# Optimization experiments

Measured on AMD Instinct MI355X. Metric: run time of the kernel, lower is better.

Reference implementation:

```python
import jax, jax.numpy as jnp
import numpy as np

N, E = 20000, 320000
NODE_DIM, HID, HEADS, OUT = 256, 64, 4, 50
NEG_SLOPE = 0.2  # PyG GATv2Conv default
BN_EPS = 1e-5


def setup_inputs() -> dict:
    key = jax.random.key(0)
    ks = jax.random.split(key, 16)
    s = 0.05
    inp = {
        'x': jax.random.normal(ks[0], (N, NODE_DIM), dtype=jnp.float32),
        'edge_index': jax.random.randint(ks[1], (2, E), 0, N, dtype=jnp.int64),
        # GATv2 layer 1: in=NODE_DIM, out=HID, heads=HEADS, concat
        'W1l': jax.random.normal(ks[2], (NODE_DIM, HEADS * HID), dtype=jnp.float32) * s,
        'W1r': jax.random.normal(ks[3], (NODE_DIM, HEADS * HID), dtype=jnp.float32) * s,
        'att1': jax.random.normal(ks[4], (HEADS, HID), dtype=jnp.float32) * s,
        'b1': jnp.zeros((HEADS * HID,), dtype=jnp.float32),
        'bn1_g': jnp.ones((HEADS * HID,), dtype=jnp.float32),
        'bn1_b': jnp.zeros((HEADS * HID,), dtype=jnp.float32),
        # GATv2 layer 2: in=HEADS*HID, out=HID, heads=1
        'W2l': jax.random.normal(ks[5], (HEADS * HID, HID), dtype=jnp.float32) * s,
        'W2r': jax.random.normal(ks[6], (HEADS * HID, HID), dtype=jnp.float32) * s,
        'att2': jax.random.normal(ks[7], (1, HID), dtype=jnp.float32) * s,
        'b2': jnp.zeros((HID,), dtype=jnp.float32),
        'bn2_g': jnp.ones((HID,), dtype=jnp.float32),
        'bn2_b': jnp.zeros((HID,), dtype=jnp.float32),
        # class head
        'Wc': jax.random.normal(ks[8], (HID, OUT), dtype=jnp.float32) * s,
        'bc': jnp.zeros((OUT,), dtype=jnp.float32),
    }
    return inp


def gatv2(x, src, dst, Wl, Wr, att, bias, heads, d):
    n = x.shape[0]
    xl = (x @ Wl).reshape(n, heads, d)  # source-side transform (messages)
    xr = (x @ Wr).reshape(n, heads, d)  # target-side transform
    xj = xl[src]                        # [E, H, D] gathered source feats
    xi = xr[dst]                        # [E, H, D] gathered target feats
    e = jax.nn.leaky_relu(xi + xj, NEG_SLOPE)
    score = jnp.einsum('ehd,hd->eh', e, att)   # [E, H]
    # segment softmax over incoming edges of each destination node
    m = jax.ops.segment_max(score, dst, num_segments=n)         # [N, H]
    m = jnp.where(jnp.isfinite(m), m, 0.0)
    p = jnp.exp(score - m[dst])
    denom = jax.ops.segment_sum(p, dst, num_segments=n)          # [N, H]
    alpha = p / (denom[dst] + 1e-16)
    out = jax.ops.segment_sum(alpha[:, :, None] * xj, dst, num_segments=n)  # [N, H, D]
    return out.reshape(n, heads * d) + bias


def batchnorm(x, gamma, beta):
    mu = jnp.mean(x, axis=0)
    var = jnp.var(x, axis=0)
    return (x - mu) * jax.lax.rsqrt(var + BN_EPS) * gamma + beta


def reference(x, edge_index, W1l, W1r, att1, b1, bn1_g, bn1_b,
              W2l, W2r, att2, b2, bn2_g, bn2_b, Wc, bc):
    src, dst = edge_index[0], edge_index[1]
    h = gatv2(x, src, dst, W1l, W1r, att1, b1, HEADS, HID)
    h = jax.nn.gelu(batchnorm(h, bn1_g, bn1_b), approximate=False)
    h = gatv2(h, src, dst, W2l, W2r, att2, b2, 1, HID)
    h = jax.nn.gelu(batchnorm(h, bn2_g, bn2_b), approximate=False)
    return jax.nn.log_softmax(h @ Wc + bc, axis=1)
```

## Files before the change

### kernel.cpp

```cpp
#include <hip/hip_runtime.h>
#include <math.h>

#define N_NODES 20000
#define N_EDGES 320000
#define NODE_DIM 256
#define HID 64
#define HEADS 4
#define OUTC 50
#define NEG_SLOPE 0.2f
#define BN_EPS 1e-5f

typedef __attribute__((ext_vector_type(8))) short short8;
typedef __attribute__((ext_vector_type(8))) unsigned short ushort8;
typedef __attribute__((ext_vector_type(4))) unsigned short ushort4v;
typedef __attribute__((ext_vector_type(4))) float f32x4;

__device__ inline unsigned short f2bf(float f) {
  unsigned u = __float_as_uint(f);
  u += 0x7fffu + ((u >> 16) & 1u);
  return (unsigned short)(u >> 16);
}

__device__ inline float bf2f(unsigned short u) {
  return __uint_as_float((unsigned)u << 16);
}

__device__ inline float gelu_exact(float v) {
  return 0.5f * v * (1.f + erff(v * 0.70710678118f));
}

__global__ void cast_f32_bf16_kernel(const float* __restrict__ in,
                                     unsigned short* __restrict__ out, int n4) {
  int i = blockIdx.x * blockDim.x + threadIdx.x;
  if (i >= n4) return;
  float4 v = ((const float4*)in)[i];
  ushort4v o = {f2bf(v.x), f2bf(v.y), f2bf(v.z), f2bf(v.w)};
  ((ushort4v*)out)[i] = o;
}

__global__ void cast_weights_kernel(const float* __restrict__ W1l, const float* __restrict__ W1r,
                                    const float* __restrict__ W2l, const float* __restrict__ W2r,
                                    unsigned short* __restrict__ w1b,
                                    unsigned short* __restrict__ w2b) {
  int i = blockIdx.x * blockDim.x + threadIdx.x;
  if (i < 131072) {
    int k = i >> 9, j = i & 511;
    w1b[i] = f2bf(j < 256 ? W1l[k * 256 + j] : W1r[k * 256 + j - 256]);
  }
  if (i < 32768) {
    int k = i >> 7, j = i & 127;
    w2b[i] = f2bf(j < 64 ? W2l[k * 64 + j] : W2r[k * 64 + j - 64]);
  }
}

__global__ __launch_bounds__(256) void gemm_bf16_kernel(
    const unsigned short* __restrict__ A, const unsigned short* __restrict__ B,
    unsigned short* __restrict__ C, int M, int K, int N) {
  __shared__ unsigned short As[128][40];
  __shared__ unsigned short Bs[64][40];
  int tid = threadIdx.x;
  int lane = tid & 63, w = tid >> 6;
  int bm = blockIdx.y * 128, bn = blockIdx.x * 64;

  f32x4 acc[2][4] = {};

  for (int k0 = 0; k0 < K; k0 += 32) {
#pragma unroll
    for (int s = tid; s < 512; s += 256) {
      int row = s >> 2, half = s & 3;
      int gr = bm + row;
      ushort8 v = {0, 0, 0, 0, 0, 0, 0, 0};
      if (gr < M) v = *(const ushort8*)&A[(size_t)gr * K + k0 + half * 8];
      *(ushort8*)&As[row][half * 8] = v;
    }
    {
      int k = tid >> 3, c0 = (tid & 7) * 8;
      ushort8 v = *(const ushort8*)&B[(size_t)(k0 + k) * N + bn + c0];
#pragma unroll
      for (int j = 0; j < 8; j++) Bs[c0 + j][k] = v[j];
    }
    __syncthreads();

    short8 av[2], bv[4];
#pragma unroll
    for (int fr = 0; fr < 2; fr++)
      av[fr] = *(const short8*)&As[w * 32 + fr * 16 + (lane & 15)][(lane >> 4) * 8];
#pragma unroll
    for (int fc = 0; fc < 4; fc++)
      bv[fc] = *(const short8*)&Bs[fc * 16 + (lane & 15)][(lane >> 4) * 8];
#pragma unroll
    for (int fr = 0; fr < 2; fr++)
#pragma unroll
      for (int fc = 0; fc < 4; fc++)
        acc[fr][fc] = __builtin_amdgcn_mfma_f32_16x16x32_bf16(av[fr], bv[fc], acc[fr][fc], 0, 0, 0);
    __syncthreads();
  }

#pragma unroll
  for (int fr = 0; fr < 2; fr++)
#pragma unroll
    for (int fc = 0; fc < 4; fc++)
#pragma unroll
      for (int i = 0; i < 4; i++) {
        int r = bm + w * 32 + fr * 16 + (lane >> 4) * 4 + i;
        if (r < M) C[(size_t)r * N + bn + fc * 16 + (lane & 15)] = f2bf(acc[fr][fc][i]);
      }
}

__global__ void hist_kernel(const int* __restrict__ dst, int* __restrict__ deg) {
  int i = blockIdx.x * blockDim.x + threadIdx.x;
  if (i < N_EDGES) atomicAdd(&deg[dst[i]], 1);
}

__global__ void scan_kernel(const int* __restrict__ deg, int* __restrict__ rowptr) {
  __shared__ int part[1024];
  int tid = threadIdx.x;
  const int CH = (N_NODES + 1023) / 1024;
  int base = tid * CH;
  int s = 0;
  for (int i = 0; i < CH; i++) {
    int idx = base + i;
    if (idx < N_NODES) s += deg[idx];
  }
  part[tid] = s;
  __syncthreads();
  for (int off = 1; off < 1024; off <<= 1) {
    int v = (tid >= off) ? part[tid - off] : 0;
    __syncthreads();
    part[tid] += v;
    __syncthreads();
  }
  int run = (tid == 0) ? 0 : part[tid - 1];
  for (int i = 0; i < CH; i++) {
    int idx = base + i;
    if (idx < N_NODES) {
      rowptr[idx] = run;
      run += deg[idx];
    }
  }
  if (tid == 1023) rowptr[N_NODES] = run;
}

__global__ void scatter_kernel(const int* __restrict__ src, const int* __restrict__ dst,
                               const int* __restrict__ rowptr, int* __restrict__ cursor,
                               int* __restrict__ csr_src) {
  int i = blockIdx.x * blockDim.x + threadIdx.x;
  if (i < N_EDGES) {
    int d = dst[i];
    int pos = rowptr[d] + atomicAdd(&cursor[d], 1);
    csr_src[pos] = src[i];
  }
}

__global__ void agg1_kernel(const unsigned short* __restrict__ C1,
                            const float* __restrict__ att, const float* __restrict__ bias,
                            const int* __restrict__ rowptr, const int* __restrict__ csr_src,
                            float* __restrict__ out) {
  int wave = threadIdx.x >> 6;
  int lane = threadIdx.x & 63;
  int n = blockIdx.x * 4 + wave;
  if (n >= N_NODES) return;

  ushort4v xi4 = *(const ushort4v*)&C1[(size_t)n * 512 + 256 + 4 * lane];
  float xi0 = bf2f(xi4[0]), xi1 = bf2f(xi4[1]), xi2 = bf2f(xi4[2]), xi3 = bf2f(xi4[3]);
  float4 attv = *(const float4*)&att[4 * lane];

  float acc0 = 0.f, acc1 = 0.f, acc2 = 0.f, acc3 = 0.f;
  float lsum = 0.f;

  int e0 = rowptr[n], e1 = rowptr[n + 1];
  int e = e0;
  for (; e + 2 <= e1; e += 2) {
    int s0 = csr_src[e];
    int s1 = csr_src[e + 1];
    ushort4v a4 = *(const ushort4v*)&C1[(size_t)s0 * 512 + 4 * lane];
    ushort4v b4 = *(const ushort4v*)&C1[(size_t)s1 * 512 + 4 * lane];
    float xa0 = bf2f(a4[0]), xa1 = bf2f(a4[1]), xa2 = bf2f(a4[2]), xa3 = bf2f(a4[3]);
    float xb0 = bf2f(b4[0]), xb1 = bf2f(b4[1]), xb2 = bf2f(b4[2]), xb3 = bf2f(b4[3]);

    float ua0 = xi0 + xa0, ua1 = xi1 + xa1, ua2 = xi2 + xa2, ua3 = xi3 + xa3;
    float ub0 = xi0 + xb0, ub1 = xi1 + xb1, ub2 = xi2 + xb2, ub3 = xi3 + xb3;
    float ta = fmaxf(ua0, NEG_SLOPE * ua0) * attv.x + fmaxf(ua1, NEG_SLOPE * ua1) * attv.y +
               fmaxf(ua2, NEG_SLOPE * ua2) * attv.z + fmaxf(ua3, NEG_SLOPE * ua3) * attv.w;
    float tb = fmaxf(ub0, NEG_SLOPE * ub0) * attv.x + fmaxf(ub1, NEG_SLOPE * ub1) * attv.y +
               fmaxf(ub2, NEG_SLOPE * ub2) * attv.z + fmaxf(ub3, NEG_SLOPE * ub3) * attv.w;

    ta += __shfl_xor(ta, 8);  tb += __shfl_xor(tb, 8);
    ta += __shfl_xor(ta, 4);  tb += __shfl_xor(tb, 4);
    ta += __shfl_xor(ta, 2);  tb += __shfl_xor(tb, 2);
    ta += __shfl_xor(ta, 1);  tb += __shfl_xor(tb, 1);

    float pa = expf(ta);
    float pb = expf(tb);
    lsum += pa + pb;
    acc0 += pa * xa0 + pb * xb0;
    acc1 += pa * xa1 + pb * xb1;
    acc2 += pa * xa2 + pb * xb2;
    acc3 += pa * xa3 + pb * xb3;
  }
  if (e < e1) {
    int s0 = csr_src[e];
    ushort4v a4 = *(const ushort4v*)&C1[(size_t)s0 * 512 + 4 * lane];
    float xa0 = bf2f(a4[0]), xa1 = bf2f(a4[1]), xa2 = bf2f(a4[2]), xa3 = bf2f(a4[3]);
    float ua0 = xi0 + xa0, ua1 = xi1 + xa1, ua2 = xi2 + xa2, ua3 = xi3 + xa3;
    float ta = fmaxf(ua0, NEG_SLOPE * ua0) * attv.x + fmaxf(ua1, NEG_SLOPE * ua1) * attv.y +
               fmaxf(ua2, NEG_SLOPE * ua2) * attv.z + fmaxf(ua3, NEG_SLOPE * ua3) * attv.w;
    ta += __shfl_xor(ta, 8);
    ta += __shfl_xor(ta, 4);
    ta += __shfl_xor(ta, 2);
    ta += __shfl_xor(ta, 1);
    float pa = expf(ta);
    lsum += pa;
    acc0 += pa * xa0;
    acc1 += pa * xa1;
    acc2 += pa * xa2;
    acc3 += pa * xa3;
  }

  float inv = 1.f / (lsum + 1e-16f);
  float4 bv = *(const float4*)&bias[4 * lane];
  float4 o;
  o.x = acc0 * inv + bv.x;
  o.y = acc1 * inv + bv.y;
  o.z = acc2 * inv + bv.z;
  o.w = acc3 * inv + bv.w;
  *(float4*)&out[(size_t)n * 256 + 4 * lane] = o;
}

__global__ void agg2_kernel(const unsigned short* __restrict__ xlr,
                            const float* __restrict__ att, const float* __restrict__ bias,
                            const int* __restrict__ rowptr, const int* __restrict__ csr_src,
                            float* __restrict__ out) {
  int wave = threadIdx.x >> 6;
  int lane = threadIdx.x & 63;
  int n = blockIdx.x * 4 + wave;
  if (n >= N_NODES) return;

  int g = lane >> 4, slot = lane & 15;
  ushort4v xi4 = *(const ushort4v*)&xlr[(size_t)n * 128 + 64 + 4 * slot];
  float xi0 = bf2f(xi4[0]), xi1 = bf2f(xi4[1]), xi2 = bf2f(xi4[2]), xi3 = bf2f(xi4[3]);
  float4 attv = *(const float4*)&att[4 * slot];

  float acc0 = 0.f, acc1 = 0.f, acc2 = 0.f, acc3 = 0.f;
  float lsum = 0.f;

  int e0 = rowptr[n], e1 = rowptr[n + 1];
  int nt = (e1 - e0 + 3) >> 2;
  for (int it = 0; it < nt; it++) {
    int e = e0 + it * 4 + g;
    bool valid = e < e1;
    int s = valid ? csr_src[e] : 0;
    ushort4v xj4 = *(const ushort4v*)&xlr[(size_t)s * 128 + 4 * slot];
    float xj0 = bf2f(xj4[0]), xj1 = bf2f(xj4[1]), xj2 = bf2f(xj4[2]), xj3 = bf2f(xj4[3]);
    float u0 = xi0 + xj0, u1 = xi1 + xj1, u2 = xi2 + xj2, u3 = xi3 + xj3;
    float t = fmaxf(u0, NEG_SLOPE * u0) * attv.x + fmaxf(u1, NEG_SLOPE * u1) * attv.y +
              fmaxf(u2, NEG_SLOPE * u2) * attv.z + fmaxf(u3, NEG_SLOPE * u3) * attv.w;
    t += __shfl_xor(t, 8);
    t += __shfl_xor(t, 4);
    t += __shfl_xor(t, 2);
    t += __shfl_xor(t, 1);
    float p = valid ? expf(t) : 0.f;
    lsum += p;
    acc0 += p * xj0;
    acc1 += p * xj1;
    acc2 += p * xj2;
    acc3 += p * xj3;
  }

  acc0 += __shfl_xor(acc0, 16); acc0 += __shfl_xor(acc0, 32);
  acc1 += __shfl_xor(acc1, 16); acc1 += __shfl_xor(acc1, 32);
  acc2 += __shfl_xor(acc2, 16); acc2 += __shfl_xor(acc2, 32);
  acc3 += __shfl_xor(acc3, 16); acc3 += __shfl_xor(acc3, 32);
  lsum += __shfl_xor(lsum, 16); lsum += __shfl_xor(lsum, 32);

  if (g == 0) {
    float inv = 1.f / (lsum + 1e-16f);
    float4 bv = *(const float4*)&bias[4 * slot];
    float4 o;
    o.x = acc0 * inv + bv.x;
    o.y = acc1 * inv + bv.y;
    o.z = acc2 * inv + bv.z;
    o.w = acc3 * inv + bv.w;
    *(float4*)&out[(size_t)n * 64 + 4 * slot] = o;
  }
}

__global__ void bn_stage1_256_kernel(const float* __restrict__ x, float* __restrict__ partial) {
  int c = threadIdx.x;
  int r0 = blockIdx.x * 84;
  int r1 = min(r0 + 84, N_NODES);
  float s = 0.f, q = 0.f;
  for (int r = r0; r < r1; r++) {
    float v = x[(size_t)r * 256 + c];
    s += v;
    q += v * v;
  }
  partial[(size_t)blockIdx.x * 512 + c] = s;
  partial[(size_t)blockIdx.x * 512 + 256 + c] = q;
}

__global__ void bn_stage1_64_kernel(const float* __restrict__ x, float* __restrict__ partial) {
  __shared__ float ls[256], lq[256];
  int tid = threadIdx.x;
  int c = tid & 63, g = tid >> 6;
  int r0 = blockIdx.x * 84 + g;
  int r1 = min(blockIdx.x * 84 + 84, N_NODES);
  float s = 0.f, q = 0.f;
  for (int r = r0; r < r1; r += 4) {
    float v = x[(size_t)r * 64 + c];
    s += v;
    q += v * v;
  }
  ls[tid] = s;
  lq[tid] = q;
  __syncthreads();
  if (g == 0) {
    s += ls[64 + c] + ls[128 + c] + ls[192 + c];
    q += lq[64 + c] + lq[128 + c] + lq[192 + c];
    partial[(size_t)blockIdx.x * 128 + c] = s;
    partial[(size_t)blockIdx.x * 128 + 64 + c] = q;
  }
}

__global__ void bn_stage2_kernel(const float* __restrict__ partial, int C,
                                 const float* __restrict__ gamma, const float* __restrict__ beta,
                                 float* __restrict__ ss) {
  int c = threadIdx.x;
  if (c >= C) return;
  float s = 0.f, q = 0.f;
  for (int b = 0; b < 240; b++) {
    s += partial[(size_t)b * 2 * C + c];
    q += partial[(size_t)b * 2 * C + C + c];
  }
  float mu = s * (1.0f / N_NODES);
  float var = q * (1.0f / N_NODES) - mu * mu;
  float sc = gamma[c] * rsqrtf(var + BN_EPS);
  ss[c] = sc;
  ss[C + c] = beta[c] - mu * sc;
}

__global__ void bn_gelu1_kernel(const float* __restrict__ x, const float* __restrict__ ss,
                                unsigned short* __restrict__ y) {
  const int total4 = N_NODES * 256 / 4;
  for (int i = blockIdx.x * blockDim.x + threadIdx.x; i < total4;
       i += gridDim.x * blockDim.x) {
    int c0 = (i & 63) * 4;
    float4 v = ((const float4*)x)[i];
    float a0 = gelu_exact(v.x * ss[c0 + 0] + ss[256 + c0 + 0]);
    float a1 = gelu_exact(v.y * ss[c0 + 1] + ss[256 + c0 + 1]);
    float a2 = gelu_exact(v.z * ss[c0 + 2] + ss[256 + c0 + 2]);
    float a3 = gelu_exact(v.w * ss[c0 + 3] + ss[256 + c0 + 3]);
    ushort4v o = {f2bf(a0), f2bf(a1), f2bf(a2), f2bf(a3)};
    ((ushort4v*)y)[i] = o;
  }
}

__global__ void bn_gelu2_kernel(const float* __restrict__ x, const float* __restrict__ ss,
                                float* __restrict__ y) {
  const int total4 = N_NODES * 64 / 4;
  for (int i = blockIdx.x * blockDim.x + threadIdx.x; i < total4;
       i += gridDim.x * blockDim.x) {
    int c0 = (i & 15) * 4;
    float4 v = ((const float4*)x)[i];
    float4 o;
    o.x = gelu_exact(v.x * ss[c0 + 0] + ss[64 + c0 + 0]);
    o.y = gelu_exact(v.y * ss[c0 + 1] + ss[64 + c0 + 1]);
    o.z = gelu_exact(v.z * ss[c0 + 2] + ss[64 + c0 + 2]);
    o.w = gelu_exact(v.w * ss[c0 + 3] + ss[64 + c0 + 3]);
    ((float4*)y)[i] = o;
  }
}

__global__ void head_kernel(const float* __restrict__ h, const float* __restrict__ Wc,
                            const float* __restrict__ bc, float* __restrict__ out) {
  __shared__ float Ws[HID * OUTC];
  __shared__ float bs[OUTC];
  for (int i = threadIdx.x; i < HID * OUTC; i += 256) Ws[i] = Wc[i];
  for (int i = threadIdx.x; i < OUTC; i += 256) bs[i] = bc[i];
  __syncthreads();

  int wave = threadIdx.x >> 6;
  int lane = threadIdx.x & 63;
  int n = blockIdx.x * 4 + wave;
  if (n >= N_NODES) return;

  float hrow = h[(size_t)n * HID + lane];
  float dot = 0.f;
#pragma unroll
  for (int k = 0; k < HID; k++) {
    float hk = __shfl(hrow, k);
    if (lane < OUTC) dot += hk * Ws[k * OUTC + lane];
  }
  float z = (lane < OUTC) ? (dot + bs[lane]) : -INFINITY;
  float mv = z;
  for (int off = 32; off; off >>= 1) mv = fmaxf(mv, __shfl_xor(mv, off));
  float p = (lane < OUTC) ? expf(z - mv) : 0.f;
  float sum = p;
  for (int off = 32; off; off >>= 1) sum += __shfl_xor(sum, off);
  if (lane < OUTC) out[(size_t)n * OUTC + lane] = z - mv - logf(sum);
}

extern "C" void kernel_launch(void* const* d_in, const int* in_sizes, int n_in,
                              void* d_out, int out_size, void* d_ws, size_t ws_size,
                              hipStream_t stream) {
  const float* x = (const float*)d_in[0];
  const int* eidx = (const int*)d_in[1];
  const float* W1l = (const float*)d_in[2];
  const float* W1r = (const float*)d_in[3];
  const float* att1 = (const float*)d_in[4];
  const float* b1 = (const float*)d_in[5];
  const float* bn1_g = (const float*)d_in[6];
  const float* bn1_b = (const float*)d_in[7];
  const float* W2l = (const float*)d_in[8];
  const float* W2r = (const float*)d_in[9];
  const float* att2 = (const float*)d_in[10];
  const float* b2 = (const float*)d_in[11];
  const float* bn2_g = (const float*)d_in[12];
  const float* bn2_b = (const float*)d_in[13];
  const float* Wc = (const float*)d_in[14];
  const float* bc = (const float*)d_in[15];
  float* out = (float*)d_out;

  const int* src = eidx;
  const int* dstv = eidx + N_EDGES;

  char* ws = (char*)d_ws;
  unsigned short* C1full = (unsigned short*)(ws + 0);
  float* out1 = (float*)(ws + 20971520);
  unsigned short* out1b = (unsigned short*)(ws + 41943040);
  unsigned short* C2full = (unsigned short*)(ws + 52428800);
  unsigned short* xb = (unsigned short*)(ws + 62914560);
  float* out2 = (float*)(ws + 62914560);
  float* partial = (float*)(ws + 73400320);
  float* ss1 = (float*)(ws + 73891840);
  float* ss2 = (float*)(ws + 73893888);
  unsigned short* w1b = (unsigned short*)(ws + 73894400);
  unsigned short* w2b = (unsigned short*)(ws + 74156544);
  int* deg = (int*)(ws + 74222080);
  int* cursor = (int*)(ws + 74302080);
  int* rowptr = (int*)(ws + 74382080);
  int* csr_src = (int*)(ws + 74462096);

  hipMemsetAsync(deg, 0, 160000, stream);

  cast_f32_bf16_kernel<<<5000, 256, 0, stream>>>(x, xb, 1280000);
  cast_weights_kernel<<<512, 256, 0, stream>>>(W1l, W1r, W2l, W2r, w1b, w2b);

  gemm_bf16_kernel<<<dim3(8, 157), 256, 0, stream>>>(xb, w1b, C1full, N_NODES, 256, 512);

  hist_kernel<<<(N_EDGES + 255) / 256, 256, 0, stream>>>(dstv, deg);
  scan_kernel<<<1, 1024, 0, stream>>>(deg, rowptr);
  scatter_kernel<<<(N_EDGES + 255) / 256, 256, 0, stream>>>(src, dstv, rowptr, cursor, csr_src);

  agg1_kernel<<<N_NODES / 4, 256, 0, stream>>>(C1full, att1, b1, rowptr, csr_src, out1);

  bn_stage1_256_kernel<<<240, 256, 0, stream>>>(out1, partial);
  bn_stage2_kernel<<<1, 256, 0, stream>>>(partial, 256, bn1_g, bn1_b, ss1);
  bn_gelu1_kernel<<<2048, 256, 0, stream>>>(out1, ss1, out1b);

  gemm_bf16_kernel<<<dim3(2, 157), 256, 0, stream>>>(out1b, w2b, C2full, N_NODES, 256, 128);

  agg2_kernel<<<N_NODES / 4, 256, 0, stream>>>(C2full, att2, b2, rowptr, csr_src, out2);

  bn_stage1_64_kernel<<<240, 256, 0, stream>>>(out2, partial);
  bn_stage2_kernel<<<1, 64, 0, stream>>>(partial, 64, bn2_g, bn2_b, ss2);
  bn_gelu2_kernel<<<1280, 256, 0, stream>>>(out2, ss2, out2);

  head_kernel<<<N_NODES / 4, 256, 0, stream>>>(out2, Wc, bc, out);
}
```

Baseline: 278.3 us.

## Fuse casts and BN-GELU into head, widen GEMM tiles, unroll agg1, use exp2

Merges the input and weight cast kernels into one launch, and folds the second BN+GELU pass into the head kernel, removing one kernel and a full read/write of the 64-wide activations. The GEMM tile grows to 128 columns with 8 MFMA fragments per wave, halving grid width. The layer-1 aggregation loop is unrolled to 4 edges, and the exponentials use exp2 with attention vectors prescaled by log2(e). The risks are higher register pressure in the GEMM and aggregation kernels and fewer GEMM blocks to spread across the GPU.

```diff
diff --git a/kernel.cpp b/kernel.cpp
--- a/kernel.cpp
+++ b/kernel.cpp
@@ -9,6 +9,7 @@
 #define OUTC 50
 #define NEG_SLOPE 0.2f
 #define BN_EPS 1e-5f
+#define LOG2E 1.4426950408889634f
 
 typedef __attribute__((ext_vector_type(8))) short short8;
 typedef __attribute__((ext_vector_type(8))) unsigned short ushort8;
@@ -29,20 +30,17 @@
   return 0.5f * v * (1.f + erff(v * 0.70710678118f));
 }
 
-__global__ void cast_f32_bf16_kernel(const float* __restrict__ in,
-                                     unsigned short* __restrict__ out, int n4) {
+__global__ void cast_all_kernel(const float* __restrict__ x, unsigned short* __restrict__ xb,
+                                const float* __restrict__ W1l, const float* __restrict__ W1r,
+                                const float* __restrict__ W2l, const float* __restrict__ W2r,
+                                unsigned short* __restrict__ w1b,
+                                unsigned short* __restrict__ w2b) {
   int i = blockIdx.x * blockDim.x + threadIdx.x;
-  if (i >= n4) return;
-  float4 v = ((const float4*)in)[i];
-  ushort4v o = {f2bf(v.x), f2bf(v.y), f2bf(v.z), f2bf(v.w)};
-  ((ushort4v*)out)[i] = o;
-}
-
-__global__ void cast_weights_kernel(const float* __restrict__ W1l, const float* __restrict__ W1r,
-                                    const float* __restrict__ W2l, const float* __restrict__ W2r,
-                                    unsigned short* __restrict__ w1b,
-                                    unsigned short* __restrict__ w2b) {
-  int i = blockIdx.x * blockDim.x + threadIdx.x;
+  if (i < 1280000) {
+    float4 v = ((const float4*)x)[i];
+    ushort4v o = {f2bf(v.x), f2bf(v.y), f2bf(v.z), f2bf(v.w)};
+    ((ushort4v*)xb)[i] = o;
+  }
   if (i < 131072) {
     int k = i >> 9, j = i & 511;
     w1b[i] = f2bf(j < 256 ? W1l[k * 256 + j] : W1r[k * 256 + j - 256]);
@@ -57,12 +55,12 @@
     const unsigned short* __restrict__ A, const unsigned short* __restrict__ B,
     unsigned short* __restrict__ C, int M, int K, int N) {
   __shared__ unsigned short As[128][40];
-  __shared__ unsigned short Bs[64][40];
+  __shared__ unsigned short Bs[128][40];
   int tid = threadIdx.x;
   int lane = tid & 63, w = tid >> 6;
-  int bm = blockIdx.y * 128, bn = blockIdx.x * 64;
-
-  f32x4 acc[2][4] = {};
+  int bm = blockIdx.y * 128, bn = blockIdx.x * 128;
+
+  f32x4 acc[2][8] = {};
 
   for (int k0 = 0; k0 < K; k0 += 32) {
 #pragma unroll
@@ -73,25 +71,26 @@
       if (gr < M) v = *(const ushort8*)&A[(size_t)gr * K + k0 + half * 8];
       *(ushort8*)&As[row][half * 8] = v;
     }
-    {
-      int k = tid >> 3, c0 = (tid & 7) * 8;
+#pragma unroll
+    for (int s = tid; s < 512; s += 256) {
+      int k = s >> 4, c0 = (s & 15) * 8;
       ushort8 v = *(const ushort8*)&B[(size_t)(k0 + k) * N + bn + c0];
 #pragma unroll
       for (int j = 0; j < 8; j++) Bs[c0 + j][k] = v[j];
     }
     __syncthreads();
 
-    short8 av[2], bv[4];
+    short8 av[2], bv[8];
 #pragma unroll
     for (int fr = 0; fr < 2; fr++)
       av[fr] = *(const short8*)&As[w * 32 + fr * 16 + (lane & 15)][(lane >> 4) * 8];
 #pragma unroll
-    for (int fc = 0; fc < 4; fc++)
+    for (int fc = 0; fc < 8; fc++)
       bv[fc] = *(const short8*)&Bs[fc * 16 + (lane & 15)][(lane >> 4) * 8];
 #pragma unroll
     for (int fr = 0; fr < 2; fr++)
 #pragma unroll
-      for (int fc = 0; fc < 4; fc++)
+      for (int fc = 0; fc < 8; fc++)
         acc[fr][fc] = __builtin_amdgcn_mfma_f32_16x16x32_bf16(av[fr], bv[fc], acc[fr][fc], 0, 0, 0);
     __syncthreads();
   }
@@ -99,7 +98,7 @@
 #pragma unroll
   for (int fr = 0; fr < 2; fr++)
 #pragma unroll
-    for (int fc = 0; fc < 4; fc++)
+    for (int fc = 0; fc < 8; fc++)
 #pragma unroll
       for (int i = 0; i < 4; i++) {
         int r = bm + w * 32 + fr * 16 + (lane >> 4) * 4 + i;
@@ -164,58 +163,69 @@
   ushort4v xi4 = *(const ushort4v*)&C1[(size_t)n * 512 + 256 + 4 * lane];
   float xi0 = bf2f(xi4[0]), xi1 = bf2f(xi4[1]), xi2 = bf2f(xi4[2]), xi3 = bf2f(xi4[3]);
   float4 attv = *(const float4*)&att[4 * lane];
+  attv.x *= LOG2E; attv.y *= LOG2E; attv.z *= LOG2E; attv.w *= LOG2E;
 
   float acc0 = 0.f, acc1 = 0.f, acc2 = 0.f, acc3 = 0.f;
   float lsum = 0.f;
 
   int e0 = rowptr[n], e1 = rowptr[n + 1];
   int e = e0;
-  for (; e + 2 <= e1; e += 2) {
-    int s0 = csr_src[e];
-    int s1 = csr_src[e + 1];
+#define EDGE_SCORE(S, T, X0, X1, X2, X3)                                              \
+  {                                                                                   \
+    float u0 = xi0 + X0, u1 = xi1 + X1, u2 = xi2 + X2, u3 = xi3 + X3;                 \
+    T = fmaxf(u0, NEG_SLOPE * u0) * attv.x + fmaxf(u1, NEG_SLOPE * u1) * attv.y +     \
+        fmaxf(u2, NEG_SLOPE * u2) * attv.z + fmaxf(u3, NEG_SLOPE * u3) * attv.w;      \
+  }
+  for (; e + 4 <= e1; e += 4) {
+    int s0 = csr_src[e], s1 = csr_src[e + 1], s2 = csr_src[e + 2], s3 = csr_src[e + 3];
     ushort4v a4 = *(const ushort4v*)&C1[(size_t)s0 * 512 + 4 * lane];
     ushort4v b4 = *(const ushort4v*)&C1[(size_t)s1 * 512 + 4 * lane];
+    ushort4v c4 = *(const ushort4v*)&C1[(size_t)s2 * 512 + 4 * lane];
+    ushort4v d4 = *(const ushort4v*)&C1[(size_t)s3 * 512 + 4 * lane];
     float xa0 = bf2f(a4[0]), xa1 = bf2f(a4[1]), xa2 = bf2f(a4[2]), xa3 = bf2f(a4[3]);
     float xb0 = bf2f(b4[0]), xb1 = bf2f(b4[1]), xb2 = bf2f(b4[2]), xb3 = bf2f(b4[3]);
-
-    float ua0 = xi0 + xa0, ua1 = xi1 + xa1, ua2 = xi2 + xa2, ua3 = xi3 + xa3;
-    float ub0 = xi0 + xb0, ub1 = xi1 + xb1, ub2 = xi2 + xb2, ub3 = xi3 + xb3;
-    float ta = fmaxf(ua0, NEG_SLOPE * ua0) * attv.x + fmaxf(ua1, NEG_SLOPE * ua1) * attv.y +
-               fmaxf(ua2, NEG_SLOPE * ua2) * attv.z + fmaxf(ua3, NEG_SLOPE * ua3) * attv.w;
-    float tb = fmaxf(ub0, NEG_SLOPE * ub0) * attv.x + fmaxf(ub1, NEG_SLOPE * ub1) * attv.y +
-               fmaxf(ub2, NEG_SLOPE * ub2) * attv.z + fmaxf(ub3, NEG_SLOPE * ub3) * attv.w;
-
-    ta += __shfl_xor(ta, 8);  tb += __shfl_xor(tb, 8);
-    ta += __shfl_xor(ta, 4);  tb += __shfl_xor(tb, 4);
-    ta += __shfl_xor(ta, 2);  tb += __shfl_xor(tb, 2);
-    ta += __shfl_xor(ta, 1);  tb += __shfl_xor(tb, 1);
-
-    float pa = expf(ta);
-    float pb = expf(tb);
-    lsum += pa + pb;
-    acc0 += pa * xa0 + pb * xb0;
-    acc1 += pa * xa1 + pb * xb1;
-    acc2 += pa * xa2 + pb * xb2;
-    acc3 += pa * xa3 + pb * xb3;
-  }
-  if (e < e1) {
+    float xc0 = bf2f(c4[0]), xc1 = bf2f(c4[1]), xc2 = bf2f(c4[2]), xc3 = bf2f(c4[3]);
+    float xd0 = bf2f(d4[0]), xd1 = bf2f(d4[1]), xd2 = bf2f(d4[2]), xd3 = bf2f(d4[3]);
+
+    float ta, tb, tc, td;
+    EDGE_SCORE(s0, ta, xa0, xa1, xa2, xa3);
+    EDGE_SCORE(s1, tb, xb0, xb1, xb2, xb3);
+    EDGE_SCORE(s2, tc, xc0, xc1, xc2, xc3);
+    EDGE_SCORE(s3, td, xd0, xd1, xd2, xd3);
+
+    ta += __shfl_xor(ta, 8); tb += __shfl_xor(tb, 8); tc += __shfl_xor(tc, 8); td += __shfl_xor(td, 8);
+    ta += __shfl_xor(ta, 4); tb += __shfl_xor(tb, 4); tc += __shfl_xor(tc, 4); td += __shfl_xor(td, 4);
+    ta += __shfl_xor(ta, 2); tb += __shfl_xor(tb, 2); tc += __shfl_xor(tc, 2); td += __shfl_xor(td, 2);
+    ta += __shfl_xor(ta, 1); tb += __shfl_xor(tb, 1); tc += __shfl_xor(tc, 1); td += __shfl_xor(td, 1);
+
+    float pa = __builtin_amdgcn_exp2f(ta);
+    float pb = __builtin_amdgcn_exp2f(tb);
+    float pc = __builtin_amdgcn_exp2f(tc);
+    float pd = __builtin_amdgcn_exp2f(td);
+    lsum += (pa + pb) + (pc + pd);
+    acc0 += pa * xa0 + pb * xb0 + pc * xc0 + pd * xd0;
+    acc1 += pa * xa1 + pb * xb1 + pc * xc1 + pd * xd1;
+    acc2 += pa * xa2 + pb * xb2 + pc * xc2 + pd * xd2;
+    acc3 += pa * xa3 + pb * xb3 + pc * xc3 + pd * xd3;
+  }
+  for (; e < e1; e++) {
     int s0 = csr_src[e];
     ushort4v a4 = *(const ushort4v*)&C1[(size_t)s0 * 512 + 4 * lane];
     float xa0 = bf2f(a4[0]), xa1 = bf2f(a4[1]), xa2 = bf2f(a4[2]), xa3 = bf2f(a4[3]);
-    float ua0 = xi0 + xa0, ua1 = xi1 + xa1, ua2 = xi2 + xa2, ua3 = xi3 + xa3;
-    float ta = fmaxf(ua0, NEG_SLOPE * ua0) * attv.x + fmaxf(ua1, NEG_SLOPE * ua1) * attv.y +
-               fmaxf(ua2, NEG_SLOPE * ua2) * attv.z + fmaxf(ua3, NEG_SLOPE * ua3) * attv.w;
+    float ta;
+    EDGE_SCORE(s0, ta, xa0, xa1, xa2, xa3);
     ta += __shfl_xor(ta, 8);
     ta += __shfl_xor(ta, 4);
     ta += __shfl_xor(ta, 2);
     ta += __shfl_xor(ta, 1);
-    float pa = expf(ta);
+    float pa = __builtin_amdgcn_exp2f(ta);
     lsum += pa;
     acc0 += pa * xa0;
     acc1 += pa * xa1;
     acc2 += pa * xa2;
     acc3 += pa * xa3;
   }
+#undef EDGE_SCORE
 
   float inv = 1.f / (lsum + 1e-16f);
   float4 bv = *(const float4*)&bias[4 * lane];
@@ -240,6 +250,7 @@
   ushort4v xi4 = *(const ushort4v*)&xlr[(size_t)n * 128 + 64 + 4 * slot];
   float xi0 = bf2f(xi4[0]), xi1 = bf2f(xi4[1]), xi2 = bf2f(xi4[2]), xi3 = bf2f(xi4[3]);
   float4 attv = *(const float4*)&att[4 * slot];
+  attv.x *= LOG2E; attv.y *= LOG2E; attv.z *= LOG2E; attv.w *= LOG2E;
 
   float acc0 = 0.f, acc1 = 0.f, acc2 = 0.f, acc3 = 0.f;
   float lsum = 0.f;
@@ -259,7 +270,7 @@
     t += __shfl_xor(t, 4);
     t += __shfl_xor(t, 2);
     t += __shfl_xor(t, 1);
-    float p = valid ? expf(t) : 0.f;
+    float p = valid ? __builtin_amdgcn_exp2f(t) : 0.f;
     lsum += p;
     acc0 += p * xj0;
     acc1 += p * xj1;
@@ -355,24 +366,9 @@
   }
 }
 
-__global__ void bn_gelu2_kernel(const float* __restrict__ x, const float* __restrict__ ss,
-                                float* __restrict__ y) {
-  const int total4 = N_NODES * 64 / 4;
-  for (int i = blockIdx.x * blockDim.x + threadIdx.x; i < total4;
-       i += gridDim.x * blockDim.x) {
-    int c0 = (i & 15) * 4;
-    float4 v = ((const float4*)x)[i];
-    float4 o;
-    o.x = gelu_exact(v.x * ss[c0 + 0] + ss[64 + c0 + 0]);
-    o.y = gelu_exact(v.y * ss[c0 + 1] + ss[64 + c0 + 1]);
-    o.z = gelu_exact(v.z * ss[c0 + 2] + ss[64 + c0 + 2]);
-    o.w = gelu_exact(v.w * ss[c0 + 3] + ss[64 + c0 + 3]);
-    ((float4*)y)[i] = o;
-  }
-}
-
-__global__ void head_kernel(const float* __restrict__ h, const float* __restrict__ Wc,
-                            const float* __restrict__ bc, float* __restrict__ out) {
+__global__ void head_kernel(const float* __restrict__ h, const float* __restrict__ ss2,
+                            const float* __restrict__ Wc, const float* __restrict__ bc,
+                            float* __restrict__ out) {
   __shared__ float Ws[HID * OUTC];
   __shared__ float bs[OUTC];
   for (int i = threadIdx.x; i < HID * OUTC; i += 256) Ws[i] = Wc[i];
@@ -384,7 +380,8 @@
   int n = blockIdx.x * 4 + wave;
   if (n >= N_NODES) return;
 
-  float hrow = h[(size_t)n * HID + lane];
+  float raw = h[(size_t)n * HID + lane];
+  float hrow = gelu_exact(raw * ss2[lane] + ss2[64 + lane]);
   float dot = 0.f;
 #pragma unroll
   for (int k = 0; k < HID; k++) {
@@ -443,10 +440,9 @@
 
   hipMemsetAsync(deg, 0, 160000, stream);
 
-  cast_f32_bf16_kernel<<<5000, 256, 0, stream>>>(x, xb, 1280000);
-  cast_weights_kernel<<<512, 256, 0, stream>>>(W1l, W1r, W2l, W2r, w1b, w2b);
-
-  gemm_bf16_kernel<<<dim3(8, 157), 256, 0, stream>>>(xb, w1b, C1full, N_NODES, 256, 512);
+  cast_all_kernel<<<5000, 256, 0, stream>>>(x, xb, W1l, W1r, W2l, W2r, w1b, w2b);
+
+  gemm_bf16_kernel<<<dim3(4, 157), 256, 0, stream>>>(xb, w1b, C1full, N_NODES, 256, 512);
 
   hist_kernel<<<(N_EDGES + 255) / 256, 256, 0, stream>>>(dstv, deg);
   scan_kernel<<<1, 1024, 0, stream>>>(deg, rowptr);
@@ -458,13 +454,12 @@
   bn_stage2_kernel<<<1, 256, 0, stream>>>(partial, 256, bn1_g, bn1_b, ss1);
   bn_gelu1_kernel<<<2048, 256, 0, stream>>>(out1, ss1, out1b);
 
-  gemm_bf16_kernel<<<dim3(2, 157), 256, 0, stream>>>(out1b, w2b, C2full, N_NODES, 256, 128);
+  gemm_bf16_kernel<<<dim3(1, 157), 256, 0, stream>>>(out1b, w2b, C2full, N_NODES, 256, 128);
 
   agg2_kernel<<<N_NODES / 4, 256, 0, stream>>>(C2full, att2, b2, rowptr, csr_src, out2);
 
   bn_stage1_64_kernel<<<240, 256, 0, stream>>>(out2, partial);
   bn_stage2_kernel<<<1, 64, 0, stream>>>(partial, 64, bn2_g, bn2_b, ss2);
-  bn_gelu2_kernel<<<1280, 256, 0, stream>>>(out2, ss2, out2);
-
-  head_kernel<<<N_NODES / 4, 256, 0, stream>>>(out2, Wc, bc, out);
-}
+
+  head_kernel<<<N_NODES / 4, 256, 0, stream>>>(out2, ss2, Wc, bc, out);
+}
```

Result: no change. 278.4 us (+0.0%).
